# Performance work log

Measured on AMD Instinct MI355X. Metric: run time of the kernel, lower is better.

The kernel has to match this reference:

```python
import jax, jax.numpy as jnp
import numpy as np

B, S, H, L = 64, 512, 768, 9


def setup_inputs() -> dict:
    key = jax.random.key(0)
    ks = jax.random.split(key, 9)
    hidden_states = jax.random.normal(ks[0], (B, S, H), dtype=jnp.float32)
    classifier_w = jax.random.normal(ks[1], (H, L), dtype=jnp.float32) * 0.02
    classifier_b = jax.random.normal(ks[2], (L,), dtype=jnp.float32) * 0.02
    class_weights = jax.random.uniform(ks[3], (L,), dtype=jnp.float32, minval=0.5, maxval=2.0)
    start_transitions = jax.random.normal(ks[4], (L,), dtype=jnp.float32) * 0.1
    end_transitions = jax.random.normal(ks[5], (L,), dtype=jnp.float32) * 0.1
    transitions = jax.random.normal(ks[6], (L, L), dtype=jnp.float32) * 0.1
    labels = jax.random.randint(ks[7], (B, S), 0, L, dtype=jnp.int64)
    special = jax.random.uniform(ks[8], (B, S)) < 0.1
    labels = jnp.where(special, jnp.asarray(-100, labels.dtype), labels)
    # variable-length sequences: attention_mask = 1 for t < length
    lengths = jax.random.randint(jax.random.fold_in(key, 7), (B,), S // 2, S + 1)
    attention_mask = (jnp.arange(S)[None, :] < lengths[:, None]).astype(jnp.int64)
    return dict(hidden_states=hidden_states, classifier_w=classifier_w,
                classifier_b=classifier_b, class_weights=class_weights,
                start_transitions=start_transitions, end_transitions=end_transitions,
                transitions=transitions, labels=labels, attention_mask=attention_mask)


def _crf_nll(emissions, tags, mask, start_transitions, end_transitions, transitions):
    """torchcrf CRF negative log-likelihood, reduction='mean', batch_first.

    emissions: (B, S, L) float; tags: (B, S) int; mask: (B, S) bool (mask[:,0] True).
    """
    Bn, Sn, Ln = emissions.shape
    maskf = mask.astype(emissions.dtype)
    batch_idx = jnp.arange(Bn)

    # ---- numerator: score of the gold tag sequence ----
    emit_tag = jnp.take_along_axis(emissions, tags[:, :, None], axis=2)[:, :, 0]  # (B,S)
    trans_score = transitions[tags[:, :-1], tags[:, 1:]]                            # (B,S-1)
    numerator = (start_transitions[tags[:, 0]] + emit_tag[:, 0]
                 + jnp.sum((trans_score + emit_tag[:, 1:]) * maskf[:, 1:], axis=1))
    last_idx = jnp.sum(mask.astype(jnp.int32), axis=1) - 1                          # (B,)
    numerator = numerator + end_transitions[tags[batch_idx, last_idx]]

    # ---- denominator: forward algorithm (log partition) ----
    score0 = start_transitions[None, :] + emissions[:, 0]                           # (B,L)

    def step(score, inp):
        emit_t, mask_t = inp                                                        # (B,L), (B,)
        # broadcast: (B, from, 1) + (from, to) + (B, 1, to)
        nxt = jax.nn.logsumexp(score[:, :, None] + transitions[None] + emit_t[:, None, :], axis=1)
        score = jnp.where(mask_t[:, None], nxt, score)
        return score, None

    emit_seq = jnp.moveaxis(emissions[:, 1:], 1, 0)   # (S-1, B, L)
    mask_seq = jnp.moveaxis(mask[:, 1:], 1, 0)        # (S-1, B)
    score, _ = jax.lax.scan(step, score0, (emit_seq, mask_seq))
    log_z = jax.nn.logsumexp(score + end_transitions[None, :], axis=1)              # (B,)

    llh = numerator - log_z
    return -jnp.mean(llh)


def reference(hidden_states, classifier_w, classifier_b, class_weights,
              start_transitions, end_transitions, transitions, labels, attention_mask):
    # Linear classifier on BERT output (dropout is identity at eval)
    emissions = jnp.einsum('bsh,hl->bsl', hidden_states, classifier_w) + classifier_b
    emissions = emissions * class_weights[None, None, :]
    # mask/label fixup as in BertCRFModel.forward
    crf_mask = (labels != -100) & (attention_mask == 1)
    crf_mask = crf_mask.at[:, 0].set(True)
    crf_labels = jnp.where(labels == -100, 0, labels)
    return _crf_nll(emissions, crf_labels, crf_mask,
                    start_transitions, end_transitions, transitions)
```

## Files before the change

kernel.cpp:

```cpp
#include <hip/hip_runtime.h>
#include <math.h>

#define Bb 64
#define Ss 512
#define Hh 768
#define Ll 9
#define CCH 32
#define TCH 16
#define NROWS (Bb * Ss)
#define NTILES (NROWS / 16)
#define KSTEPS 24
#define KHALF 12
#define EST 12
#define EMIS_SMEM 28672
#define CRF_SMEM  14336

typedef __attribute__((ext_vector_type(8))) short short8;
typedef __attribute__((ext_vector_type(4))) float f32x4;

__device__ __forceinline__ ushort f2bf(float f) {
    unsigned u = __float_as_uint(f);
    return (ushort)((u + 0x7FFFu + ((u >> 16) & 1u)) >> 16);
}
__device__ __forceinline__ float uniform_sgpr(float x) {
    return __int_as_float(__builtin_amdgcn_readfirstlane(__float_as_int(x)));
}

__global__ __launch_bounds__(512, 2) void k_emis(
    const float* __restrict__ hs, const float* __restrict__ W,
    const float* __restrict__ bvec, const float* __restrict__ cw,
    float* __restrict__ ee2, float* __restrict__ out)
{
    extern __shared__ char smem[];
    uint4* bpack = (uint4*)smem;
    float* comb  = (float*)(smem + 24576);
    const int tid = threadIdx.x;

    if (blockIdx.x == 0 && tid == 0) out[0] = 0.f;

    const int wid  = tid >> 6;
    const int tl   = wid >> 1;
    const int half = wid & 1;
    const int lane = tid & 63;
    const int col = lane & 15, kg = lane >> 4;
    const int gtile = blockIdx.x * 4 + tl;
    const int row0 = gtile * 16;
    const float* ap = hs + (size_t)(row0 + col) * Hh + kg * 8 + half * (KHALF * 32);

    float4 c0[4], c1[4];
#pragma unroll
    for (int p = 0; p < 4; ++p) {
        c0[p] = *(const float4*)(ap + p * 32);
        c1[p] = *(const float4*)(ap + p * 32 + 4);
    }

    for (int slot = tid; slot < KSTEPS * 64; slot += 512) {
        const int s = slot >> 6, l = slot & 63;
        const int bcol = l & 15, bkg = l >> 4;
        ushort h[8];
#pragma unroll
        for (int j = 0; j < 8; ++j) {
            const int k = s * 32 + bkg * 8 + j;
            h[j] = (bcol < Ll) ? f2bf(W[k * Ll + bcol]) : (ushort)0;
        }
        uint4 u;
        u.x = (unsigned)h[0] | ((unsigned)h[1] << 16);
        u.y = (unsigned)h[2] | ((unsigned)h[3] << 16);
        u.z = (unsigned)h[4] | ((unsigned)h[5] << 16);
        u.w = (unsigned)h[6] | ((unsigned)h[7] << 16);
        bpack[slot] = u;
    }
    __syncthreads();

    f32x4 acc = {0.f, 0.f, 0.f, 0.f};
#pragma unroll
    for (int t = 0; t < KHALF; ++t) {
        const int sl = t & 3;
        const float4 a0 = c0[sl], a1 = c1[sl];
        if (t + 4 < KHALF) {
            c0[sl] = *(const float4*)(ap + (t + 4) * 32);
            c1[sl] = *(const float4*)(ap + (t + 4) * 32 + 4);
        }
        const unsigned x0 = __float_as_uint(a0.x), x1 = __float_as_uint(a0.y);
        const unsigned x2 = __float_as_uint(a0.z), x3 = __float_as_uint(a0.w);
        const unsigned y0 = __float_as_uint(a1.x), y1 = __float_as_uint(a1.y);
        const unsigned y2 = __float_as_uint(a1.z), y3 = __float_as_uint(a1.w);
        uint4 au;
        au.x = (x1 & 0xFFFF0000u) | (x0 >> 16);
        au.y = (x3 & 0xFFFF0000u) | (x2 >> 16);
        au.z = (y1 & 0xFFFF0000u) | (y0 >> 16);
        au.w = (y3 & 0xFFFF0000u) | (y2 >> 16);
        const short8 a = __builtin_bit_cast(short8, au);
        const short8 b = __builtin_bit_cast(short8,
                                            bpack[(half * KHALF + t) * 64 + lane]);
        acc = __builtin_amdgcn_mfma_f32_16x16x32_bf16(a, b, acc, 0, 0, 0);
    }

    if (half == 1) {
#pragma unroll
        for (int j = 0; j < 4; ++j)
            comb[(tl * 4 + j) * 64 + lane] = acc[j];
    }
    __syncthreads();
    if (half == 0) {
#pragma unroll
        for (int j = 0; j < 4; ++j)
            acc[j] += comb[(tl * 4 + j) * 64 + lane];
        if (col < Ll) {
            const float cwv = cw[col], bv = bvec[col];
#pragma unroll
            for (int j = 0; j < 4; ++j)
                ee2[(size_t)(row0 + kg * 4 + j) * EST + col] =
                    __expf((acc[j] + bv) * cwv);
        }
    }
}

__global__ __launch_bounds__(384) void k_crf(
    const float* __restrict__ ee2, const int* __restrict__ labels,
    const int* __restrict__ attn, const float* __restrict__ trans,
    const float* __restrict__ startt, const float* __restrict__ endt,
    float* __restrict__ out)
{
    extern __shared__ char smem[];
    int*   mkt_s    = (int*)smem;
    float* trans_s  = (float*)(smem + 2048);
    float* et_s     = (float*)(smem + 2372);
    float* erow_s   = (float*)(smem + 2696);
    float* rowmax_s = (float*)(smem + 13064);
    float* num_s    = (float*)(smem + 14216);

    const int b   = blockIdx.x;
    const int tid = threadIdx.x;

    for (int t = tid; t < Ss; t += 384) {
        const int lab = labels[b * Ss + t];
        const int att = attn[b * Ss + t];
        const int tag = (lab == -100) ? 0 : lab;
        const int mk  = ((lab != -100) && (att == 1)) ? 1 : 0;
        mkt_s[t] = tag | (mk << 4);
    }
    if (tid < Ll * Ll) {
        const float tv = trans[tid];
        trans_s[tid] = tv;
        et_s[tid] = __expf(tv);
    }
    __syncthreads();

    if (tid < CCH * Ll) {
        const int i = tid % Ll;
        const int c = tid / Ll;
        float et[Ll][Ll];
#pragma unroll
        for (int l = 0; l < Ll; ++l)
#pragma unroll
            for (int k = 0; k < Ll; ++k)
                et[l][k] = uniform_sgpr(et_s[l * Ll + k]);

        const float* ep = ee2 + (size_t)(b * Ss + c * TCH) * EST;
        float4 p0[2], p1[2]; float p2[2];
        p0[0] = *(const float4*)ep;
        p1[0] = *(const float4*)(ep + 4);
        p2[0] = ep[8];

        float u[Ll];
#pragma unroll
        for (int l = 0; l < Ll; ++l) u[l] = (l == i) ? 1.f : 0.f;
        float rlog = 0.f;

#pragma unroll
        for (int s = 0; s < TCH; ++s) {
            const int cur = s & 1;
            if (s + 1 < TCH) {
                const float* np = ep + (s + 1) * EST;
                p0[cur ^ 1] = *(const float4*)np;
                p1[cur ^ 1] = *(const float4*)(np + 4);
                p2[cur ^ 1] = np[8];
            }
            const int t = c * TCH + s;
            const int mv = mkt_s[t];
            if ((c != 0 || s > 0) && (mv >> 4)) {
                float e[Ll];
                e[0] = p0[cur].x; e[1] = p0[cur].y; e[2] = p0[cur].z; e[3] = p0[cur].w;
                e[4] = p1[cur].x; e[5] = p1[cur].y; e[6] = p1[cur].z; e[7] = p1[cur].w;
                e[8] = p2[cur];
                float nu[Ll];
#pragma unroll
                for (int k = 0; k < Ll; ++k) {
                    float sacc = 0.f;
#pragma unroll
                    for (int l = 0; l < Ll; ++l) sacc = fmaf(u[l], et[l][k], sacc);
                    nu[k] = sacc * e[k];
                }
#pragma unroll
                for (int l = 0; l < Ll; ++l) u[l] = nu[l];
            }
            if ((s & 3) == 3) {
                float mx = u[0];
#pragma unroll
                for (int l = 1; l < Ll; ++l) mx = fmaxf(mx, u[l]);
                rlog += __logf(mx);
                const float r = 1.f / mx;
#pragma unroll
                for (int l = 0; l < Ll; ++l) u[l] *= r;
            }
        }
        float mx = u[0];
#pragma unroll
        for (int l = 1; l < Ll; ++l) mx = fmaxf(mx, u[l]);
        rowmax_s[c * Ll + i] = rlog + __logf(mx);
        const float r = 1.f / mx;
#pragma unroll
        for (int l = 0; l < Ll; ++l)
            erow_s[(c * Ll + i) * Ll + l] = u[l] * r;
    }

    if (tid >= 320) {
        const int lane = tid - 320;
        float psum = 0.f;
        int pcnt = 0;
        for (int t = lane; t < Ss; t += 64) {
            const int mv  = mkt_s[t];
            const int tag = mv & 15;
            const bool mk = (mv >> 4) || (t == 0);
            if (t >= 1 && (mv >> 4)) {
                const int tagp = mkt_s[t - 1] & 15;
                psum += trans_s[tagp * Ll + tag] +
                        __logf(ee2[(size_t)(b * Ss + t) * EST + tag]);
            }
            pcnt += mk ? 1 : 0;
        }
#pragma unroll
        for (int off = 32; off; off >>= 1) {
            psum += __shfl_xor(psum, off);
            pcnt += __shfl_xor(pcnt, off);
        }
        if (lane == 0) {
            const int tag0 = mkt_s[0] & 15;
            const int tagL = mkt_s[pcnt - 1] & 15;
            num_s[0] = startt[tag0] + __logf(ee2[(size_t)(b * Ss) * EST + tag0])
                       + psum + endt[tagL];
        }
    }
    __syncthreads();

    if (tid < Ll) {
        const int lane = tid;
        float sc[Ll];
#pragma unroll
        for (int l = 0; l < Ll; ++l)
            sc[l] = startt[l] + __logf(ee2[(size_t)(b * Ss) * EST + l]);
        for (int c = 0; c < CCH; ++c) {
            float u[Ll];
#pragma unroll
            for (int l = 0; l < Ll; ++l) u[l] = sc[l] + rowmax_s[c * Ll + l];
            float M = u[0];
#pragma unroll
            for (int l = 1; l < Ll; ++l) M = fmaxf(M, u[l]);
            float sacc = 0.f;
#pragma unroll
            for (int l = 0; l < Ll; ++l)
                sacc = fmaf(__expf(u[l] - M), erow_s[(c * Ll + l) * Ll + lane], sacc);
            const float ns = M + __logf(sacc);
#pragma unroll
            for (int l = 0; l < Ll; ++l) sc[l] = __shfl(ns, l);
        }
        float M2 = sc[0] + endt[0];
#pragma unroll
        for (int l = 1; l < Ll; ++l) M2 = fmaxf(M2, sc[l] + endt[l]);
        float s2 = 0.f;
#pragma unroll
        for (int l = 0; l < Ll; ++l) s2 += __expf(sc[l] + endt[l] - M2);
        if (lane == 0) {
            const float logz = M2 + __logf(s2);
            atomicAdd(out, -(num_s[0] - logz) * (1.f / Bb));
        }
    }
}

extern "C" void kernel_launch(void* const* d_in, const int* in_sizes, int n_in,
                              void* d_out, int out_size, void* d_ws, size_t ws_size,
                              hipStream_t stream)
{
    const float* hs     = (const float*)d_in[0];
    const float* W      = (const float*)d_in[1];
    const float* bvec   = (const float*)d_in[2];
    const float* cw     = (const float*)d_in[3];
    const float* startt = (const float*)d_in[4];
    const float* endt   = (const float*)d_in[5];
    const float* trans  = (const float*)d_in[6];
    const int*   labels = (const int*)d_in[7];
    const int*   attn   = (const int*)d_in[8];
    float* out = (float*)d_out;
    float* ee2 = (float*)d_ws;

    hipLaunchKernelGGL(k_emis, dim3(NTILES / 4), dim3(512), EMIS_SMEM, stream,
                       hs, W, bvec, cw, ee2, out);
    hipLaunchKernelGGL(k_crf, dim3(Bb), dim3(384), CRF_SMEM, stream,
                       ee2, labels, attn, trans, startt, endt, out);
}
```

Before: 44.35 us.

## Replace serial CRF chunk combine with parallel tree reduction of transfer matrices

The final sequential pass over 32 chunk transfer matrices, run by 9 threads, is replaced with a 5-level binary tree. Each level multiplies pairs of normalized 9x9 matrices in parallel, keeping log row-scales, and ping-pongs between two shared-memory buffers. The numerator loop is also unrolled and multiplies emission exponentials before taking logs, so it needs fewer log calls. This shortens the serial tail of the CRF kernel but adds block-wide barriers and more shared memory, and the product of exponentials can underflow or overflow.

New measurement: 42.30 us. 1.05x faster.

```diff
diff --git a/kernel.cpp b/kernel.cpp
--- a/kernel.cpp
+++ b/kernel.cpp
@@ -13,7 +13,7 @@
 #define KHALF 12
 #define EST 12
 #define EMIS_SMEM 28672
-#define CRF_SMEM  14336
+#define CRF_SMEM  20480
 
 typedef __attribute__((ext_vector_type(8))) short short8;
 typedef __attribute__((ext_vector_type(4))) float f32x4;
@@ -123,12 +123,14 @@
     float* __restrict__ out)
 {
     extern __shared__ char smem[];
-    int*   mkt_s    = (int*)smem;
-    float* trans_s  = (float*)(smem + 2048);
-    float* et_s     = (float*)(smem + 2372);
-    float* erow_s   = (float*)(smem + 2696);
-    float* rowmax_s = (float*)(smem + 13064);
-    float* num_s    = (float*)(smem + 14216);
+    int*   mkt_s   = (int*)smem;
+    float* trans_s = (float*)(smem + 2048);
+    float* et_s    = (float*)(smem + 2372);
+    float* rm0     = (float*)(smem + 2696);
+    float* er0     = (float*)(smem + 3848);
+    float* rm1     = (float*)(smem + 14216);
+    float* er1     = (float*)(smem + 14792);
+    float* num_s   = (float*)(smem + 19976);
 
     const int b   = blockIdx.x;
     const int tid = threadIdx.x;
@@ -208,28 +210,32 @@
         float mx = u[0];
 #pragma unroll
         for (int l = 1; l < Ll; ++l) mx = fmaxf(mx, u[l]);
-        rowmax_s[c * Ll + i] = rlog + __logf(mx);
+        rm0[c * Ll + i] = rlog + __logf(mx);
         const float r = 1.f / mx;
 #pragma unroll
         for (int l = 0; l < Ll; ++l)
-            erow_s[(c * Ll + i) * Ll + l] = u[l] * r;
+            er0[(c * Ll + i) * Ll + l] = u[l] * r;
     }
 
     if (tid >= 320) {
         const int lane = tid - 320;
-        float psum = 0.f;
+        float psum = 0.f, pr0 = 1.f, pr1 = 1.f;
         int pcnt = 0;
-        for (int t = lane; t < Ss; t += 64) {
+#pragma unroll
+        for (int j = 0; j < 8; ++j) {
+            const int t = lane + j * 64;
             const int mv  = mkt_s[t];
             const int tag = mv & 15;
             const bool mk = (mv >> 4) || (t == 0);
             if (t >= 1 && (mv >> 4)) {
                 const int tagp = mkt_s[t - 1] & 15;
-                psum += trans_s[tagp * Ll + tag] +
-                        __logf(ee2[(size_t)(b * Ss + t) * EST + tag]);
+                psum += trans_s[tagp * Ll + tag];
+                const float ev = ee2[(size_t)(b * Ss + t) * EST + tag];
+                if (j < 4) pr0 *= ev; else pr1 *= ev;
             }
             pcnt += mk ? 1 : 0;
         }
+        psum += __logf(pr0) + __logf(pr1);
 #pragma unroll
         for (int off = 32; off; off >>= 1) {
             psum += __shfl_xor(psum, off);
@@ -242,39 +248,69 @@
                        + psum + endt[tagL];
         }
     }
+
+    float *rs = rm0, *es = er0, *rd = rm1, *ed = er1;
+    int nodes = 16;
+    for (int lev = 0; lev < 5; ++lev) {
+        __syncthreads();
+        if (tid < nodes * Ll) {
+            const int node = tid / Ll, i = tid % Ll;
+            const float* rmA = rs + (2 * node) * Ll;
+            const float* erA = es + (size_t)(2 * node) * Ll * Ll;
+            const float* rmB = rs + (2 * node + 1) * Ll;
+            const float* erB = es + (size_t)(2 * node + 1) * Ll * Ll;
+            float MB = rmB[0];
+#pragma unroll
+            for (int l = 1; l < Ll; ++l) MB = fmaxf(MB, rmB[l]);
+            float w[Ll];
+#pragma unroll
+            for (int l = 0; l < Ll; ++l)
+                w[l] = erA[i * Ll + l] * __expf(rmB[l] - MB);
+            float p[Ll];
+#pragma unroll
+            for (int k = 0; k < Ll; ++k) {
+                float s = 0.f;
+#pragma unroll
+                for (int l = 0; l < Ll; ++l) s = fmaf(w[l], erB[l * Ll + k], s);
+                p[k] = s;
+            }
+            float pm = p[0];
+#pragma unroll
+            for (int k = 1; k < Ll; ++k) pm = fmaxf(pm, p[k]);
+            pm = fmaxf(pm, 1e-30f);
+            rd[node * Ll + i] = rmA[i] + MB + __logf(pm);
+            const float r = 1.f / pm;
+#pragma unroll
+            for (int k = 0; k < Ll; ++k)
+                ed[node * Ll * Ll + i * Ll + k] = p[k] * r;
+        }
+        float* t1 = rs; rs = rd; rd = t1;
+        float* t2 = es; es = ed; ed = t2;
+        nodes >>= 1;
+    }
     __syncthreads();
 
-    if (tid < Ll) {
-        const int lane = tid;
-        float sc[Ll];
-#pragma unroll
-        for (int l = 0; l < Ll; ++l)
-            sc[l] = startt[l] + __logf(ee2[(size_t)(b * Ss) * EST + l]);
-        for (int c = 0; c < CCH; ++c) {
-            float u[Ll];
-#pragma unroll
-            for (int l = 0; l < Ll; ++l) u[l] = sc[l] + rowmax_s[c * Ll + l];
-            float M = u[0];
-#pragma unroll
-            for (int l = 1; l < Ll; ++l) M = fmaxf(M, u[l]);
-            float sacc = 0.f;
-#pragma unroll
-            for (int l = 0; l < Ll; ++l)
-                sacc = fmaf(__expf(u[l] - M), erow_s[(c * Ll + l) * Ll + lane], sacc);
-            const float ns = M + __logf(sacc);
-#pragma unroll
-            for (int l = 0; l < Ll; ++l) sc[l] = __shfl(ns, l);
-        }
-        float M2 = sc[0] + endt[0];
-#pragma unroll
-        for (int l = 1; l < Ll; ++l) M2 = fmaxf(M2, sc[l] + endt[l]);
-        float s2 = 0.f;
-#pragma unroll
-        for (int l = 0; l < Ll; ++l) s2 += __expf(sc[l] + endt[l] - M2);
-        if (lane == 0) {
-            const float logz = M2 + __logf(s2);
-            atomicAdd(out, -(num_s[0] - logz) * (1.f / Bb));
-        }
+    if (tid == 0) {
+        const float* rmT = rs;
+        const float* erT = es;
+        float g[Ll];
+        float MG = -1e30f;
+#pragma unroll
+        for (int l = 0; l < Ll; ++l) {
+            g[l] = startt[l] + __logf(ee2[(size_t)(b * Ss) * EST + l]) + rmT[l];
+            MG = fmaxf(MG, g[l]);
+        }
+        float tot = 0.f;
+#pragma unroll
+        for (int k = 0; k < Ll; ++k) {
+            float vk = 0.f;
+#pragma unroll
+            for (int i = 0; i < Ll; ++i)
+                vk = fmaf(__expf(g[i] - MG), erT[i * Ll + k], vk);
+            tot += vk * __expf(endt[k]);
+        }
+        const float logz = MG + __logf(tot);
+        atomicAdd(out, -(num_s[0] - logz) * (1.f / Bb));
     }
 }
 
```
